# Kernel tuning notes

Hardware: AMD Instinct MI355X
Metric: run time of the kernel (lower is better)

Reference implementation:

```python
import jax, jax.numpy as jnp
import numpy as np

B, I, H = 16384, 1024, 1024

def setup_inputs() -> dict:
    key = jax.random.key(0)
    ks = jax.random.split(key, 7)
    scale = 0.02  # small init so gates are not saturated
    return {
        "x": jax.random.normal(ks[0], (B, I), jnp.float32),
        "h_prev": jax.random.normal(ks[1], (B, H), jnp.float32),
        "c_prev": jax.random.normal(ks[2], (B, H), jnp.float32),
        "Wx": jax.random.normal(ks[3], (4, H, I), jnp.float32) * scale,  # order: z,i,f,o
        "bx": jnp.zeros((4, H), jnp.float32),
        "Rh": jax.random.normal(ks[4], (4, H, H), jnp.float32) * scale,
        "bh": jnp.zeros((4, H), jnp.float32),
    }

def reference(x, h_prev, c_prev, Wx, bx, Rh, bh):
    # Fused form of 4 input-GEMMs + 4 recurrent-GEMMs: two einsums over stacked gates.
    # gate order g=0..3 -> z, i, f, o
    pre = (jnp.einsum('bi,ghi->bgh', x, Wx) + bx[None]
           + jnp.einsum('bh,gkh->bgk', h_prev, Rh) + bh[None])  # [B,4,H]
    z = jnp.tanh(pre[:, 0])
    i = jax.nn.sigmoid(pre[:, 1])
    f = jax.nn.sigmoid(pre[:, 2])
    o = jax.nn.sigmoid(pre[:, 3])
    c = f * c_prev + i * z
    h = o * jnp.tanh(c)
    return (h, c)
```

## Files before the change

kernel.cpp:

```cpp
#include <hip/hip_runtime.h>
#include <hip/hip_bf16.h>
#include <stdint.h>


typedef __attribute__((ext_vector_type(8))) short bf16x8;
typedef __attribute__((ext_vector_type(4))) float f32x4;
typedef __attribute__((ext_vector_type(8))) unsigned short u16x8;

#define AS1 __attribute__((address_space(1)))
#define AS3 __attribute__((address_space(3)))

constexpr int BATCH = 16384;
constexpr int HDIM  = 1024;
constexpr int KDIM  = 2048;
constexpr int NDIM  = 4096;

__device__ inline unsigned short f2bf(float f) {
  uint32_t u = __builtin_bit_cast(uint32_t, f);
  u += 0x7fffu + ((u >> 16) & 1u);
  return (unsigned short)(u >> 16);
}
__device__ inline u16x8 cvt8(const float* __restrict__ src) {
  float4 f0 = *(const float4*)src;
  float4 f1 = *(const float4*)(src + 4);
  u16x8 v;
  v[0] = f2bf(f0.x); v[1] = f2bf(f0.y); v[2] = f2bf(f0.z); v[3] = f2bf(f0.w);
  v[4] = f2bf(f1.x); v[5] = f2bf(f1.y); v[6] = f2bf(f1.z); v[7] = f2bf(f1.w);
  return v;
}
__device__ inline float sigmoid_f(float x) {
  float e = __builtin_amdgcn_exp2f(-1.4426950408889634f * x);
  return __builtin_amdgcn_rcpf(1.0f + e);
}
__device__ inline float tanh_f(float x) {
  float e = __builtin_amdgcn_exp2f(2.8853900817779268f * x);
  return 1.0f - 2.0f * __builtin_amdgcn_rcpf(1.0f + e);
}

__global__ void pack_xh(const float* __restrict__ x, const float* __restrict__ hp,
                        unsigned short* __restrict__ xh) {
  const int64_t nch = (int64_t)BATCH * KDIM / 8;
  for (int64_t c = (int64_t)blockIdx.x * blockDim.x + threadIdx.x; c < nch;
       c += (int64_t)gridDim.x * blockDim.x) {
    const int b = (int)(c >> 8);
    const int k = ((int)c & 255) * 8;
    const float* src = (k < 1024) ? (x + (int64_t)b * 1024 + k)
                                  : (hp + (int64_t)b * 1024 + (k - 1024));
    *(u16x8*)(xh + c * 8) = cvt8(src);
  }
}
__global__ void pack_w(const float* __restrict__ Wx, const float* __restrict__ Rh,
                       unsigned short* __restrict__ wp) {
  const int64_t nch = (int64_t)NDIM * KDIM / 8;
  for (int64_t c = (int64_t)blockIdx.x * blockDim.x + threadIdx.x; c < nch;
       c += (int64_t)gridDim.x * blockDim.x) {
    const int np = (int)(c >> 8);
    const int k = ((int)c & 255) * 8;
    const int h = np >> 2, g = np & 3;
    const float* src = (k < 1024) ? (Wx + (int64_t)(g * HDIM + h) * 1024 + k)
                                  : (Rh + (int64_t)(g * HDIM + h) * 1024 + (k - 1024));
    *(u16x8*)(wp + c * 8) = cvt8(src);
  }
}
__global__ void pack_bias(const float* __restrict__ bx, const float* __restrict__ bh,
                          float* __restrict__ bias) {
  int n = blockIdx.x * blockDim.x + threadIdx.x;
  if (n < NDIM) {
    int h = n >> 2, g = n & 3;
    bias[n] = bx[g * HDIM + h] + bh[g * HDIM + h];
  }
}

template <int OFF>
__device__ __forceinline__ bf16x8 dsb128(uint32_t a) {
  bf16x8 r;
  asm volatile("ds_read_b128 %0, %1 offset:%2" : "=v"(r) : "v"(a), "i"(OFF) : "memory");
  return r;
}

#define BARR    asm volatile("s_barrier" ::: "memory")
#define LGKM12  asm volatile("s_waitcnt lgkmcnt(12)" ::: "memory")
#define VM8     asm volatile("s_waitcnt vmcnt(8)" ::: "memory")
#define VM0     asm volatile("s_waitcnt vmcnt(0)" ::: "memory")
#define SCHED0  __builtin_amdgcn_sched_barrier(0)

#define ISS_A8(FA, BUF, KH) { constexpr int _o = (BUF)*32768 + (KH)*16384;   \
  FA[0] = dsb128<_o>(av);      FA[1] = dsb128<_o+1024>(av);                   \
  FA[2] = dsb128<_o+2048>(av); FA[3] = dsb128<_o+3072>(av);                   \
  FA[4] = dsb128<_o+4096>(av); FA[5] = dsb128<_o+5120>(av);                   \
  FA[6] = dsb128<_o+6144>(av); FA[7] = dsb128<_o+7168>(av); }
#define ISS_B4(FB, BUF, KH) { constexpr int _o = (BUF)*32768 + (KH)*16384;   \
  FB[0] = dsb128<_o>(bv);      FB[1] = dsb128<_o+1024>(bv);                   \
  FB[2] = dsb128<_o+2048>(bv); FB[3] = dsb128<_o+3072>(bv); }

#define MFMA32(FA, FB) { \
  __builtin_amdgcn_s_setprio(1); \
  _Pragma("unroll") for (int mh = 0; mh < 2; ++mh) \
  _Pragma("unroll") for (int mi = 0; mi < 4; ++mi) \
  _Pragma("unroll") for (int ni = 0; ni < 4; ++ni) \
    acc[mh * 4 + mi][ni] = __builtin_amdgcn_mfma_f32_16x16x32_bf16(FA[mh * 4 + mi], FB[ni], acc[mh * 4 + mi][ni], 0, 0, 0); \
  __builtin_amdgcn_s_setprio(0); }

#define STAGE(SRC, DOFF) { \
  __builtin_amdgcn_global_load_lds((const AS1 void*)(SRC), (AS3 void*)(dstL + (DOFF)), 16, 0, 0); \
  __builtin_amdgcn_global_load_lds((const AS1 void*)((SRC) + 524288), (AS3 void*)(dstL + (DOFF) + 8192), 16, 0, 0); }

__global__ __launch_bounds__(512, 2) void lstm_gemm(
    const unsigned short* __restrict__ XH, const unsigned short* __restrict__ Wp,
    const float* __restrict__ bias, const float* __restrict__ c_prev,
    float* __restrict__ out_h, float* __restrict__ out_c) {
  __shared__ __align__(1024) char smem_[131072];

  const int tid  = threadIdx.x;
  const int l    = tid & 63;
  const int w    = tid >> 6;
  const int wr   = w >> 2, wc = w & 3;
  const int la   = l & 15;
  const int kg   = l >> 4;

  const int xcd = blockIdx.x & 7;
  const int q   = blockIdx.x >> 3;
  const int tn  = xcd * 2 + (q & 1);
  const int tm  = q >> 1;
  const int m0  = tm * 256;
  const int n0  = tn * 256;

  const int rbase = w * 16 + (l >> 2);
  const int ck    = (l & 3) ^ ((l >> 3) & 3);
  const char* pA = (const char*)XH + (int64_t)(m0 + rbase) * 4096 + ck * 16;
  const char* pB = (const char*)Wp + (int64_t)(n0 + rbase) * 4096 + ck * 16;
  char* dstL = smem_ + w * 1024;

  const int cc = kg ^ ((la >> 1) & 3);
  const uint32_t lds0 = (uint32_t)(uintptr_t)(AS3 char*)smem_;
  const uint32_t av = lds0 + wr * 8192 + la * 64 + cc * 16;
  const uint32_t bv = lds0 + 65536 + wc * 4096 + la * 64 + cc * 16;

  f32x4 acc[8][4] = {};
  bf16x8 fa0[8], fa1[8], fb0[4], fb1[4];

  STAGE(pB,       65536);
  STAGE(pA,       0);
  STAGE(pB + 64,  81920);
  STAGE(pA + 64,  16384);
  STAGE(pB + 128, 98304);
  STAGE(pA + 128, 32768);
  VM8; BARR;
  ISS_B4(fb0, 0, 0) ISS_A8(fa0, 0, 0)

#pragma unroll 1
  for (int it = 0; it < 16; ++it) {
    int kt2 = 2 * it + 2; if (kt2 > 31) kt2 = 31;
    int kt3 = 2 * it + 3; if (kt3 > 31) kt3 = 31;
    const char* sB1 = pB + (2 * it + 1) * 128;
    const char* sA1 = pA + (2 * it + 1) * 128;
    const char* sA2 = pA + kt2 * 128;
    const char* sA3 = pA + kt3 * 128;
    const char* sB2 = pB + kt2 * 128;
    const char* sB3 = pB + kt3 * 128;

    BARR;
    STAGE(sB1 + 64, 114688);
    STAGE(sA1 + 64, 49152);
    VM8;
    ISS_B4(fb1, 0, 1) ISS_A8(fa1, 0, 1)
    LGKM12; SCHED0; MFMA32(fa0, fb0)

    BARR;
    STAGE(sB2, 65536);
    STAGE(sA2, 0);
    VM8;
    ISS_B4(fb0, 1, 0) ISS_A8(fa0, 1, 0)
    LGKM12; SCHED0; MFMA32(fa1, fb1)

    BARR;
    STAGE(sB2 + 64, 81920);
    STAGE(sA2 + 64, 16384);
    VM8;
    ISS_B4(fb1, 1, 1) ISS_A8(fa1, 1, 1)
    LGKM12; SCHED0; MFMA32(fa0, fb0)

    BARR;
    STAGE(sB3, 98304);
    STAGE(sA3, 32768);
    VM8;
    ISS_B4(fb0, 0, 0) ISS_A8(fa0, 0, 0)
    LGKM12; SCHED0; MFMA32(fa1, fb1)
  }

  VM0;
  __syncthreads();
  float* ew = (float*)smem_ + w * 1088;
  const float4 bias4 = *(const float4*)(bias + n0 + wc * 64 + 4 * la);
  const int hg = ((n0 + wc * 64) >> 2) + la;

#pragma unroll
  for (int mi = 0; mi < 8; ++mi) {
#pragma unroll
    for (int ni = 0; ni < 4; ++ni)
#pragma unroll
      for (int r = 0; r < 4; ++r)
        ew[(4 * kg + r) * 68 + ni * 16 + la] = acc[mi][ni][r];
#pragma unroll
    for (int p = 0; p < 4; ++p) {
      const int row = p * 4 + kg;
      float4 g4 = *(const float4*)(ew + row * 68 + 4 * la);
      const int b = m0 + wr * 128 + mi * 16 + row;
      const uint32_t oidx = (uint32_t)b * HDIM + (uint32_t)hg;
      const float cp = c_prev[oidx];
      const float zg = tanh_f(g4.x + bias4.x);
      const float ig = sigmoid_f(g4.y + bias4.y);
      const float fg = sigmoid_f(g4.z + bias4.z);
      const float og = sigmoid_f(g4.w + bias4.w);
      const float cn = fg * cp + ig * zg;
      out_h[oidx] = og * tanh_f(cn);
      out_c[oidx] = cn;
    }
  }
}

extern "C" void kernel_launch(void* const* d_in, const int* in_sizes, int n_in,
                              void* d_out, int out_size, void* d_ws, size_t ws_size,
                              hipStream_t stream) {
  const float* x  = (const float*)d_in[0];
  const float* hp = (const float*)d_in[1];
  const float* cp = (const float*)d_in[2];
  const float* Wx = (const float*)d_in[3];
  const float* bx = (const float*)d_in[4];
  const float* Rh = (const float*)d_in[5];
  const float* bh = (const float*)d_in[6];

  unsigned short* XH = (unsigned short*)d_ws;
  unsigned short* Wp = XH + (size_t)BATCH * KDIM;
  float* bias = (float*)(Wp + (size_t)NDIM * KDIM);
  float* out_h = (float*)d_out;
  float* out_c = out_h + (size_t)BATCH * HDIM;

  pack_xh<<<2048, 256, 0, stream>>>(x, hp, XH);
  pack_w<<<1024, 256, 0, stream>>>(Wx, Rh, Wp);
  pack_bias<<<16, 256, 0, stream>>>(bx, bh, bias);
  lstm_gemm<<<1024, 512, 0, stream>>>(XH, Wp, bias, cp, out_h, out_c);
}
```

Measured before the change: 316.6 us.

## Load B fragments directly from global in MFMA-fragment layout, drop B LDS staging

The weight packing kernel now writes W in the exact per-lane MFMA fragment order, so each wave can load its B fragments straight from global memory into registers with 16-byte vector loads. This skips staging B through LDS, halving shared memory to 64KB and removing the B ds_reads. Wait counts are retuned to match the new mix of global and LDS operations. The trade-off is that B fragments are no longer shared across waves through LDS, so each wave re-reads them from global or L2, and global-load latency now sits directly in front of the MFMAs.

Measured after the change: 324.3 us. +2.4%, slower.

```diff
diff --git a/kernel.cpp b/kernel.cpp
--- a/kernel.cpp
+++ b/kernel.cpp
@@ -49,13 +49,19 @@
     *(u16x8*)(xh + c * 8) = cvt8(src);
   }
 }
+
 __global__ void pack_w(const float* __restrict__ Wx, const float* __restrict__ Rh,
                        unsigned short* __restrict__ wp) {
   const int64_t nch = (int64_t)NDIM * KDIM / 8;
   for (int64_t c = (int64_t)blockIdx.x * blockDim.x + threadIdx.x; c < nch;
        c += (int64_t)gridDim.x * blockDim.x) {
-    const int np = (int)(c >> 8);
-    const int k = ((int)c & 255) * 8;
+    const int l   = (int)c & 63;
+    const int ni  = ((int)c >> 6) & 3;
+    const int kk  = ((int)c >> 8) & 63;
+    const int c64 = (int)(c >> 14);
+    const int la = l & 15, kg = l >> 4;
+    const int np = c64 * 64 + ni * 16 + la;
+    const int k  = kk * 32 + kg * 8;
     const int h = np >> 2, g = np & 3;
     const float* src = (k < 1024) ? (Wx + (int64_t)(g * HDIM + h) * 1024 + k)
                                   : (Rh + (int64_t)(g * HDIM + h) * 1024 + (k - 1024));
@@ -79,8 +85,9 @@
 }
 
 #define BARR    asm volatile("s_barrier" ::: "memory")
-#define LGKM12  asm volatile("s_waitcnt lgkmcnt(12)" ::: "memory")
-#define VM8     asm volatile("s_waitcnt vmcnt(8)" ::: "memory")
+#define LGKM8   asm volatile("s_waitcnt lgkmcnt(8)" ::: "memory")
+#define VM6     asm volatile("s_waitcnt vmcnt(6)" ::: "memory")
+#define VM4     asm volatile("s_waitcnt vmcnt(4)" ::: "memory")
 #define VM0     asm volatile("s_waitcnt vmcnt(0)" ::: "memory")
 #define SCHED0  __builtin_amdgcn_sched_barrier(0)
 
@@ -89,9 +96,10 @@
   FA[2] = dsb128<_o+2048>(av); FA[3] = dsb128<_o+3072>(av);                   \
   FA[4] = dsb128<_o+4096>(av); FA[5] = dsb128<_o+5120>(av);                   \
   FA[6] = dsb128<_o+6144>(av); FA[7] = dsb128<_o+7168>(av); }
-#define ISS_B4(FB, BUF, KH) { constexpr int _o = (BUF)*32768 + (KH)*16384;   \
-  FB[0] = dsb128<_o>(bv);      FB[1] = dsb128<_o+1024>(bv);                   \
-  FB[2] = dsb128<_o+2048>(bv); FB[3] = dsb128<_o+3072>(bv); }
+
+#define BLOAD4(FB, BP) { \
+  FB[0] = *(const bf16x8*)((BP));        FB[1] = *(const bf16x8*)((BP) + 1024); \
+  FB[2] = *(const bf16x8*)((BP) + 2048); FB[3] = *(const bf16x8*)((BP) + 3072); }
 
 #define MFMA32(FA, FB) { \
   __builtin_amdgcn_s_setprio(1); \
@@ -109,7 +117,7 @@
     const unsigned short* __restrict__ XH, const unsigned short* __restrict__ Wp,
     const float* __restrict__ bias, const float* __restrict__ c_prev,
     float* __restrict__ out_h, float* __restrict__ out_c) {
-  __shared__ __align__(1024) char smem_[131072];
+  __shared__ __align__(1024) char smem_[65536];
 
   const int tid  = threadIdx.x;
   const int l    = tid & 63;
@@ -128,64 +136,64 @@
   const int rbase = w * 16 + (l >> 2);
   const int ck    = (l & 3) ^ ((l >> 3) & 3);
   const char* pA = (const char*)XH + (int64_t)(m0 + rbase) * 4096 + ck * 16;
-  const char* pB = (const char*)Wp + (int64_t)(n0 + rbase) * 4096 + ck * 16;
   char* dstL = smem_ + w * 1024;
 
   const int cc = kg ^ ((la >> 1) & 3);
   const uint32_t lds0 = (uint32_t)(uintptr_t)(AS3 char*)smem_;
   const uint32_t av = lds0 + wr * 8192 + la * 64 + cc * 16;
-  const uint32_t bv = lds0 + 65536 + wc * 4096 + la * 64 + cc * 16;
+
+  const char* pBw = (const char*)Wp + (int64_t)(tn * 4 + wc) * 262144 + l * 16;
 
   f32x4 acc[8][4] = {};
   bf16x8 fa0[8], fa1[8], fb0[4], fb1[4];
 
-  STAGE(pB,       65536);
   STAGE(pA,       0);
-  STAGE(pB + 64,  81920);
   STAGE(pA + 64,  16384);
-  STAGE(pB + 128, 98304);
   STAGE(pA + 128, 32768);
-  VM8; BARR;
-  ISS_B4(fb0, 0, 0) ISS_A8(fa0, 0, 0)
+  BLOAD4(fb0, pBw)
+  VM4; BARR;
+  ISS_A8(fa0, 0, 0)
 
 #pragma unroll 1
   for (int it = 0; it < 16; ++it) {
     int kt2 = 2 * it + 2; if (kt2 > 31) kt2 = 31;
     int kt3 = 2 * it + 3; if (kt3 > 31) kt3 = 31;
-    const char* sB1 = pB + (2 * it + 1) * 128;
+    int kk4 = 4 * it + 4; if (kk4 > 63) kk4 = 63;
     const char* sA1 = pA + (2 * it + 1) * 128;
     const char* sA2 = pA + kt2 * 128;
     const char* sA3 = pA + kt3 * 128;
-    const char* sB2 = pB + kt2 * 128;
-    const char* sB3 = pB + kt3 * 128;
-
-    BARR;
-    STAGE(sB1 + 64, 114688);
+    const char* b1 = pBw + (int64_t)(4 * it + 1) * 4096;
+    const char* b2 = pBw + (int64_t)(4 * it + 2) * 4096;
+    const char* b3 = pBw + (int64_t)(4 * it + 3) * 4096;
+    const char* b4 = pBw + (int64_t)kk4 * 4096;
+
+    BARR;
     STAGE(sA1 + 64, 49152);
-    VM8;
-    ISS_B4(fb1, 0, 1) ISS_A8(fa1, 0, 1)
-    LGKM12; SCHED0; MFMA32(fa0, fb0)
-
-    BARR;
-    STAGE(sB2, 65536);
+    BLOAD4(fb1, b1)
+    VM6;
+    ISS_A8(fa1, 0, 1)
+    LGKM8; SCHED0; MFMA32(fa0, fb0)
+
+    BARR;
     STAGE(sA2, 0);
-    VM8;
-    ISS_B4(fb0, 1, 0) ISS_A8(fa0, 1, 0)
-    LGKM12; SCHED0; MFMA32(fa1, fb1)
-
-    BARR;
-    STAGE(sB2 + 64, 81920);
+    BLOAD4(fb0, b2)
+    VM6;
+    ISS_A8(fa0, 1, 0)
+    LGKM8; SCHED0; MFMA32(fa1, fb1)
+
+    BARR;
     STAGE(sA2 + 64, 16384);
-    VM8;
-    ISS_B4(fb1, 1, 1) ISS_A8(fa1, 1, 1)
-    LGKM12; SCHED0; MFMA32(fa0, fb0)
-
-    BARR;
-    STAGE(sB3, 98304);
+    BLOAD4(fb1, b3)
+    VM6;
+    ISS_A8(fa1, 1, 1)
+    LGKM8; SCHED0; MFMA32(fa0, fb0)
+
+    BARR;
     STAGE(sA3, 32768);
-    VM8;
-    ISS_B4(fb0, 0, 0) ISS_A8(fa0, 0, 0)
-    LGKM12; SCHED0; MFMA32(fa1, fb1)
+    BLOAD4(fb0, b4)
+    VM6;
+    ISS_A8(fa0, 0, 0)
+    LGKM8; SCHED0; MFMA32(fa1, fb1)
   }
 
   VM0;
```

## Restructure GEMM to 16 waves with 4-slot single-k-half LDS ring

Applied to the files above, without the earlier changes.

The block grows from 512 to 1024 threads, so each wave owns a 64x64 output tile instead of 128x64. The K pipeline becomes a 4-slot ring of 32-wide k-slices prefetched two slices ahead, replacing the two double-buffered k-halves. Each step now waits for all LDS reads to finish before its MFMAs, relying on other waves rather than in-wave overlap to hide latency. The intent is more waves to hide latency and fewer accumulator registers per wave, at the cost of more LDS reads per MFMA and more barriers per unit of math.

Measured after the change: 310.1 us. 2.0% less time.

```diff
diff --git a/kernel.cpp b/kernel.cpp
--- a/kernel.cpp
+++ b/kernel.cpp
@@ -79,33 +79,40 @@
 }
 
 #define BARR    asm volatile("s_barrier" ::: "memory")
-#define LGKM12  asm volatile("s_waitcnt lgkmcnt(12)" ::: "memory")
-#define VM8     asm volatile("s_waitcnt vmcnt(8)" ::: "memory")
+#define LGKM0   asm volatile("s_waitcnt lgkmcnt(0)" ::: "memory")
+#define VM2     asm volatile("s_waitcnt vmcnt(2)" ::: "memory")
 #define VM0     asm volatile("s_waitcnt vmcnt(0)" ::: "memory")
 #define SCHED0  __builtin_amdgcn_sched_barrier(0)
 
-#define ISS_A8(FA, BUF, KH) { constexpr int _o = (BUF)*32768 + (KH)*16384;   \
-  FA[0] = dsb128<_o>(av);      FA[1] = dsb128<_o+1024>(av);                   \
-  FA[2] = dsb128<_o+2048>(av); FA[3] = dsb128<_o+3072>(av);                   \
-  FA[4] = dsb128<_o+4096>(av); FA[5] = dsb128<_o+5120>(av);                   \
-  FA[6] = dsb128<_o+6144>(av); FA[7] = dsb128<_o+7168>(av); }
-#define ISS_B4(FB, BUF, KH) { constexpr int _o = (BUF)*32768 + (KH)*16384;   \
-  FB[0] = dsb128<_o>(bv);      FB[1] = dsb128<_o+1024>(bv);                   \
-  FB[2] = dsb128<_o+2048>(bv); FB[3] = dsb128<_o+3072>(bv); }
-
-#define MFMA32(FA, FB) { \
+#define ISS(SLOT) { \
+  fa[0] = dsb128<(SLOT)*16384>(av);        fa[1] = dsb128<(SLOT)*16384 + 1024>(av); \
+  fa[2] = dsb128<(SLOT)*16384 + 2048>(av); fa[3] = dsb128<(SLOT)*16384 + 3072>(av); \
+  fb[0] = dsb128<(SLOT)*16384>(bv);        fb[1] = dsb128<(SLOT)*16384 + 1024>(bv); \
+  fb[2] = dsb128<(SLOT)*16384 + 2048>(bv); fb[3] = dsb128<(SLOT)*16384 + 3072>(bv); }
+
+#define MFMA16 { \
   __builtin_amdgcn_s_setprio(1); \
-  _Pragma("unroll") for (int mh = 0; mh < 2; ++mh) \
   _Pragma("unroll") for (int mi = 0; mi < 4; ++mi) \
   _Pragma("unroll") for (int ni = 0; ni < 4; ++ni) \
-    acc[mh * 4 + mi][ni] = __builtin_amdgcn_mfma_f32_16x16x32_bf16(FA[mh * 4 + mi], FB[ni], acc[mh * 4 + mi][ni], 0, 0, 0); \
+    acc[mi][ni] = __builtin_amdgcn_mfma_f32_16x16x32_bf16(fa[mi], fb[ni], acc[mi][ni], 0, 0, 0); \
   __builtin_amdgcn_s_setprio(0); }
 
-#define STAGE(SRC, DOFF) { \
-  __builtin_amdgcn_global_load_lds((const AS1 void*)(SRC), (AS3 void*)(dstL + (DOFF)), 16, 0, 0); \
-  __builtin_amdgcn_global_load_lds((const AS1 void*)((SRC) + 524288), (AS3 void*)(dstL + (DOFF) + 8192), 16, 0, 0); }
-
-__global__ __launch_bounds__(512, 2) void lstm_gemm(
+#define STAGE(JS, SLOT) { \
+  __builtin_amdgcn_global_load_lds((const AS1 void*)(pA + (int64_t)(JS) * 64), \
+      (AS3 void*)(smem_ + (SLOT)*16384 + dstOff), 16, 0, 0); \
+  __builtin_amdgcn_global_load_lds((const AS1 void*)(pB + (int64_t)(JS) * 64), \
+      (AS3 void*)(smem_ + 65536 + (SLOT)*16384 + dstOff), 16, 0, 0); }
+
+#define BODY(B, SLOT, SLOT2) { \
+  BARR; \
+  int js = 4 * it + (B) + 2; if (js > 63) js = 63; \
+  STAGE(js, SLOT2) \
+  ISS(SLOT) \
+  LGKM0; SCHED0; \
+  MFMA16 \
+  VM2; }
+
+__global__ __launch_bounds__(1024, 4) void lstm_gemm(
     const unsigned short* __restrict__ XH, const unsigned short* __restrict__ Wp,
     const float* __restrict__ bias, const float* __restrict__ c_prev,
     float* __restrict__ out_h, float* __restrict__ out_c) {
@@ -129,63 +136,26 @@
   const int ck    = (l & 3) ^ ((l >> 3) & 3);
   const char* pA = (const char*)XH + (int64_t)(m0 + rbase) * 4096 + ck * 16;
   const char* pB = (const char*)Wp + (int64_t)(n0 + rbase) * 4096 + ck * 16;
-  char* dstL = smem_ + w * 1024;
+  const int dstOff = w * 1024;
 
   const int cc = kg ^ ((la >> 1) & 3);
   const uint32_t lds0 = (uint32_t)(uintptr_t)(AS3 char*)smem_;
-  const uint32_t av = lds0 + wr * 8192 + la * 64 + cc * 16;
+  const uint32_t av = lds0 + wr * 4096 + la * 64 + cc * 16;
   const uint32_t bv = lds0 + 65536 + wc * 4096 + la * 64 + cc * 16;
 
-  f32x4 acc[8][4] = {};
-  bf16x8 fa0[8], fa1[8], fb0[4], fb1[4];
-
-  STAGE(pB,       65536);
-  STAGE(pA,       0);
-  STAGE(pB + 64,  81920);
-  STAGE(pA + 64,  16384);
-  STAGE(pB + 128, 98304);
-  STAGE(pA + 128, 32768);
-  VM8; BARR;
-  ISS_B4(fb0, 0, 0) ISS_A8(fa0, 0, 0)
+  f32x4 acc[4][4] = {};
+  bf16x8 fa[4], fb[4];
+
+  STAGE(0, 0)
+  STAGE(1, 1)
+  VM2;
 
 #pragma unroll 1
   for (int it = 0; it < 16; ++it) {
-    int kt2 = 2 * it + 2; if (kt2 > 31) kt2 = 31;
-    int kt3 = 2 * it + 3; if (kt3 > 31) kt3 = 31;
-    const char* sB1 = pB + (2 * it + 1) * 128;
-    const char* sA1 = pA + (2 * it + 1) * 128;
-    const char* sA2 = pA + kt2 * 128;
-    const char* sA3 = pA + kt3 * 128;
-    const char* sB2 = pB + kt2 * 128;
-    const char* sB3 = pB + kt3 * 128;
-
-    BARR;
-    STAGE(sB1 + 64, 114688);
-    STAGE(sA1 + 64, 49152);
-    VM8;
-    ISS_B4(fb1, 0, 1) ISS_A8(fa1, 0, 1)
-    LGKM12; SCHED0; MFMA32(fa0, fb0)
-
-    BARR;
-    STAGE(sB2, 65536);
-    STAGE(sA2, 0);
-    VM8;
-    ISS_B4(fb0, 1, 0) ISS_A8(fa0, 1, 0)
-    LGKM12; SCHED0; MFMA32(fa1, fb1)
-
-    BARR;
-    STAGE(sB2 + 64, 81920);
-    STAGE(sA2 + 64, 16384);
-    VM8;
-    ISS_B4(fb1, 1, 1) ISS_A8(fa1, 1, 1)
-    LGKM12; SCHED0; MFMA32(fa0, fb0)
-
-    BARR;
-    STAGE(sB3, 98304);
-    STAGE(sA3, 32768);
-    VM8;
-    ISS_B4(fb0, 0, 0) ISS_A8(fa0, 0, 0)
-    LGKM12; SCHED0; MFMA32(fa1, fb1)
+    BODY(0, 0, 2)
+    BODY(1, 1, 3)
+    BODY(2, 2, 0)
+    BODY(3, 3, 1)
   }
 
   VM0;
@@ -195,7 +165,7 @@
   const int hg = ((n0 + wc * 64) >> 2) + la;
 
 #pragma unroll
-  for (int mi = 0; mi < 8; ++mi) {
+  for (int mi = 0; mi < 4; ++mi) {
 #pragma unroll
     for (int ni = 0; ni < 4; ++ni)
 #pragma unroll
@@ -205,7 +175,7 @@
     for (int p = 0; p < 4; ++p) {
       const int row = p * 4 + kg;
       float4 g4 = *(const float4*)(ew + row * 68 + 4 * la);
-      const int b = m0 + wr * 128 + mi * 16 + row;
+      const int b = m0 + wr * 64 + mi * 16 + row;
       const uint32_t oidx = (uint32_t)b * HDIM + (uint32_t)hg;
       const float cp = c_prev[oidx];
       const float zg = tanh_f(g4.x + bias4.x);
@@ -239,5 +209,5 @@
   pack_xh<<<2048, 256, 0, stream>>>(x, hp, XH);
   pack_w<<<1024, 256, 0, stream>>>(Wx, Rh, Wp);
   pack_bias<<<16, 256, 0, stream>>>(bx, bh, bias);
-  lstm_gemm<<<1024, 512, 0, stream>>>(XH, Wp, bias, cp, out_h, out_c);
-}
+  lstm_gemm<<<1024, 1024, 0, stream>>>(XH, Wp, bias, cp, out_h, out_c);
+}
```
